# Kernel tuning notes

Hardware: AMD Instinct MI355X
Metric: run time of the kernel (lower is better)

The kernel has to match this reference:

```python
import jax, jax.numpy as jnp
import numpy as np

N_NODES = 100000
N_EDGES = 1600000
IN_DIM = 128
HID = 128
OUT = 40


def setup_inputs() -> dict:
    key = jax.random.key(0)
    ks = jax.random.split(key, 8)
    x = jax.random.normal(ks[0], (N_NODES, IN_DIM), dtype=jnp.float32)
    edge_index = jax.random.randint(ks[1], (2, N_EDGES), 0, N_NODES, dtype=jnp.int64)
    def glorot(k, fan_in, fan_out):
        s = jnp.sqrt(6.0 / (fan_in + fan_out)).astype(jnp.float32)
        return jax.random.uniform(k, (fan_in, fan_out), jnp.float32, -s, s)
    return {
        "x": x,
        "edge_index": edge_index,
        "W1": glorot(ks[2], IN_DIM, HID), "b1": jnp.zeros((HID,), jnp.float32),
        "W2": glorot(ks[3], HID, HID),    "b2": jnp.zeros((HID,), jnp.float32),
        "W3": glorot(ks[4], HID, HID),    "b3": jnp.zeros((HID,), jnp.float32),
        "Wl": glorot(ks[5], HID, OUT),    "bl": jnp.zeros((OUT,), jnp.float32),
    }


def _gcn_norm(edge_index, num_nodes):
    # PyG GCNConv default: add self-loops, symmetric normalization.
    loops = jnp.arange(num_nodes, dtype=edge_index.dtype)
    src = jnp.concatenate([edge_index[0], loops])
    dst = jnp.concatenate([edge_index[1], loops])
    deg = jax.ops.segment_sum(jnp.ones_like(dst, dtype=jnp.float32), dst,
                              num_segments=num_nodes)
    dis = jnp.where(deg > 0, jax.lax.rsqrt(deg), 0.0)  # deg^{-1/2}
    norm = dis[src] * dis[dst]  # [E+N]
    return src, dst, norm


def _gcn_conv(x, W, b, src, dst, norm, num_nodes):
    h = x @ W                                   # [N, F_out]
    msg = h[src] * norm[:, None]                # gather + scale
    out = jax.ops.segment_sum(msg, dst, num_segments=num_nodes)
    return out + b


def reference(x, edge_index, W1, b1, W2, b2, W3, b3, Wl, bl):
    n = x.shape[0]
    src, dst, norm = _gcn_norm(edge_index, n)
    h = jax.nn.relu(_gcn_conv(x, W1, b1, src, dst, norm, n))
    h = jax.nn.relu(_gcn_conv(h, W2, b2, src, dst, norm, n))
    h = _gcn_conv(h, W3, b3, src, dst, norm, n)
    # dropout p=0.5 is identity in eval mode
    return h @ Wl + bl
```

## Files before the change

### kernel.cpp

```cpp
#include <hip/hip_runtime.h>

typedef __attribute__((ext_vector_type(8))) short sh8;
typedef __attribute__((ext_vector_type(4))) float f4;

__device__ __forceinline__ float bf2f(unsigned short u) {
    union { unsigned int u; float f; } c; c.u = ((unsigned int)u) << 16; return c.f;
}
__device__ __forceinline__ unsigned short f2bf(float f) {
    union { float f; unsigned int u; } c; c.f = f;
    unsigned int x = c.u;
    unsigned int r = (x + 0x7fffu + ((x >> 16) & 1u)) >> 16;
    return (unsigned short)r;
}
__device__ __forceinline__ void bfsplit(float x, short& hi, short& lo) {
    unsigned short h = f2bf(x);
    float r = x - bf2f(h);
    hi = (short)h;
    lo = (short)f2bf(r);
}

__global__ void k_zero_cnt(int* cnt, int N) {
    int i = blockIdx.x * 256 + threadIdx.x;
    if (i < N) cnt[i] = 0;
}

__global__ void k_count(const int* __restrict__ dst, int* __restrict__ cnt, int E, int N) {
    int g = blockIdx.x & 7;
    int j = blockIdx.x >> 3;
    int nb = gridDim.x >> 3;
    int lo = (int)((long long)g * N / 8);
    int hi = (int)((long long)(g + 1) * N / 8);
    for (int e = j * 256 + threadIdx.x; e < E; e += nb * 256) {
        int d = dst[e];
        if (d >= lo && d < hi) atomicAdd(&cnt[d], 1);
    }
}

#define SCAN_B 256
__global__ void k_scan_a(const int* __restrict__ cnt, int* __restrict__ rowptr,
                         int* __restrict__ bsum, float* __restrict__ dis, int N) {
    __shared__ int sh[SCAN_B];
    int t = threadIdx.x, i = blockIdx.x * SCAN_B + t;
    int v = (i < N) ? cnt[i] : 0;
    if (i < N) dis[i] = rsqrtf((float)(v + 1));
    sh[t] = v; __syncthreads();
    for (int off = 1; off < SCAN_B; off <<= 1) {
        int x = (t >= off) ? sh[t - off] : 0;
        __syncthreads();
        sh[t] += x;
        __syncthreads();
    }
    int incl = sh[t];
    if (i < N) rowptr[i] = incl - v;
    if (t == SCAN_B - 1) bsum[blockIdx.x] = incl;
}

__global__ void k_scan_b(int* bsum, int NB) {
    __shared__ int sh[512];
    int t = threadIdx.x;
    int v = (t < NB) ? bsum[t] : 0;
    sh[t] = v; __syncthreads();
    for (int off = 1; off < 512; off <<= 1) {
        int x = (t >= off) ? sh[t - off] : 0;
        __syncthreads();
        sh[t] += x;
        __syncthreads();
    }
    if (t < NB) bsum[t] = sh[t] - v;
}

__global__ void k_scan_c(int* __restrict__ rowptr, int* __restrict__ cursor,
                         const int* __restrict__ bsum, int N) {
    int i = blockIdx.x * 256 + threadIdx.x;
    if (i < N) {
        int r = rowptr[i] + bsum[blockIdx.x];
        rowptr[i] = r;
        cursor[i] = r;
    }
}

__global__ void k_fill(const int* __restrict__ src, const int* __restrict__ dst,
                       int* __restrict__ cursor, int* __restrict__ csrc, int E, int N) {
    int g = blockIdx.x & 7;
    int j = blockIdx.x >> 3;
    int nb = gridDim.x >> 3;
    int lo = (int)((long long)g * N / 8);
    int hi = (int)((long long)(g + 1) * N / 8);
    for (int e = j * 256 + threadIdx.x; e < E; e += nb * 256) {
        int d = dst[e];
        if (d < lo || d >= hi) continue;
        int s = src[e];
        if ((unsigned)s >= (unsigned)N) continue;
        int p = atomicAdd(&cursor[d], 1);
        csrc[p] = s;
    }
}

__global__ __launch_bounds__(256)
void k_gemm128_a32(const float* __restrict__ X,
                   const float* __restrict__ W,
                   unsigned short* __restrict__ H, int nPairs) {
    int wave = threadIdx.x >> 6;
    int lane = threadIdx.x & 63;
    int ln = lane & 15, quad = lane >> 4;
    int c0 = (wave & 1) * 64;
    int subTile = wave >> 1;

    sh8 bh[4][4], blo[4][4];
    #pragma unroll
    for (int nt = 0; nt < 4; ++nt) {
        int col = c0 + nt * 16 + ln;
        #pragma unroll
        for (int kt = 0; kt < 4; ++kt) {
            int k0 = kt * 32 + quad * 8;
            #pragma unroll
            for (int j = 0; j < 8; ++j) {
                short h, l;
                bfsplit(W[(k0 + j) * 128 + col], h, l);
                bh[nt][kt][j] = h; blo[nt][kt][j] = l;
            }
        }
    }

    for (int p = blockIdx.x; p < nPairs; p += gridDim.x) {
        int nodeBase = p * 32 + subTile * 16;
        const float* xrow = X + (nodeBase + ln) * 128 + quad * 8;
        sh8 ah[4], al[4];
        #pragma unroll
        for (int kt = 0; kt < 4; ++kt) {
            f4 v0 = *(const f4*)(xrow + kt * 32);
            f4 v1 = *(const f4*)(xrow + kt * 32 + 4);
            #pragma unroll
            for (int j = 0; j < 4; ++j) {
                short h, l;
                bfsplit(v0[j], h, l); ah[kt][j] = h; al[kt][j] = l;
                bfsplit(v1[j], h, l); ah[kt][j + 4] = h; al[kt][j + 4] = l;
            }
        }

        f4 acc[4] = { {0.f,0.f,0.f,0.f}, {0.f,0.f,0.f,0.f}, {0.f,0.f,0.f,0.f}, {0.f,0.f,0.f,0.f} };
        #pragma unroll
        for (int kt = 0; kt < 4; ++kt)
            #pragma unroll
            for (int nt = 0; nt < 4; ++nt) {
                acc[nt] = __builtin_amdgcn_mfma_f32_16x16x32_bf16(ah[kt], bh[nt][kt], acc[nt], 0, 0, 0);
                acc[nt] = __builtin_amdgcn_mfma_f32_16x16x32_bf16(ah[kt], blo[nt][kt], acc[nt], 0, 0, 0);
                acc[nt] = __builtin_amdgcn_mfma_f32_16x16x32_bf16(al[kt], bh[nt][kt], acc[nt], 0, 0, 0);
            }

        #pragma unroll
        for (int nt = 0; nt < 4; ++nt) {
            int col = c0 + nt * 16 + ln;
            #pragma unroll
            for (int r = 0; r < 4; ++r)
                H[(nodeBase + quad * 4 + r) * 128 + col] = f2bf(acc[nt][r]);
        }
    }
}

__global__ __launch_bounds__(256)
void k_gemm128_a16(const unsigned short* __restrict__ X,
                   const float* __restrict__ W,
                   unsigned short* __restrict__ H, int nPairs) {
    int wave = threadIdx.x >> 6;
    int lane = threadIdx.x & 63;
    int ln = lane & 15, quad = lane >> 4;
    int c0 = (wave & 1) * 64;
    int subTile = wave >> 1;

    sh8 bh[4][4], blo[4][4];
    #pragma unroll
    for (int nt = 0; nt < 4; ++nt) {
        int col = c0 + nt * 16 + ln;
        #pragma unroll
        for (int kt = 0; kt < 4; ++kt) {
            int k0 = kt * 32 + quad * 8;
            #pragma unroll
            for (int j = 0; j < 8; ++j) {
                short h, l;
                bfsplit(W[(k0 + j) * 128 + col], h, l);
                bh[nt][kt][j] = h; blo[nt][kt][j] = l;
            }
        }
    }

    for (int p = blockIdx.x; p < nPairs; p += gridDim.x) {
        int nodeBase = p * 32 + subTile * 16;
        const unsigned short* xrow = X + (nodeBase + ln) * 128 + quad * 8;
        sh8 a[4];
        #pragma unroll
        for (int kt = 0; kt < 4; ++kt) a[kt] = *(const sh8*)(xrow + kt * 32);

        f4 acc[4] = { {0.f,0.f,0.f,0.f}, {0.f,0.f,0.f,0.f}, {0.f,0.f,0.f,0.f}, {0.f,0.f,0.f,0.f} };
        #pragma unroll
        for (int kt = 0; kt < 4; ++kt)
            #pragma unroll
            for (int nt = 0; nt < 4; ++nt) {
                acc[nt] = __builtin_amdgcn_mfma_f32_16x16x32_bf16(a[kt], bh[nt][kt], acc[nt], 0, 0, 0);
                acc[nt] = __builtin_amdgcn_mfma_f32_16x16x32_bf16(a[kt], blo[nt][kt], acc[nt], 0, 0, 0);
            }

        #pragma unroll
        for (int nt = 0; nt < 4; ++nt) {
            int col = c0 + nt * 16 + ln;
            #pragma unroll
            for (int r = 0; r < 4; ++r)
                H[(nodeBase + quad * 4 + r) * 128 + col] = f2bf(acc[nt][r]);
        }
    }
}

__global__ __launch_bounds__(256)
void k_agg(const unsigned short* __restrict__ H,
           unsigned short* __restrict__ O,
           const float* __restrict__ dis,
           const int* __restrict__ rowptr,
           const int* __restrict__ cnt,
           const int* __restrict__ csrc,
           const float* __restrict__ bias,
           int relu, int N) {
    int n = (blockIdx.x * 256 + threadIdx.x) >> 6;
    int lane = threadIdx.x & 63;
    if (n >= N) return;
    int c = lane * 2;

    float dn = dis[n];
    unsigned int hv = *(const unsigned int*)(H + n * 128 + c);
    float a0 = bf2f((unsigned short)hv) * dn * dn;
    float a1 = bf2f((unsigned short)(hv >> 16)) * dn * dn;

    int start = rowptr[n];
    int e = cnt[n];
    int i = 0;
    for (; i + 8 <= e; i += 8) {
        int s[8];
        #pragma unroll
        for (int q = 0; q < 8; ++q) s[q] = csrc[start + i + q];
        unsigned int v[8];
        #pragma unroll
        for (int q = 0; q < 8; ++q) v[q] = *(const unsigned int*)(H + (size_t)s[q] * 128 + c);
        float w[8];
        #pragma unroll
        for (int q = 0; q < 8; ++q) w[q] = dis[s[q]] * dn;
        #pragma unroll
        for (int q = 0; q < 8; ++q) {
            a0 += w[q] * bf2f((unsigned short)v[q]);
            a1 += w[q] * bf2f((unsigned short)(v[q] >> 16));
        }
    }
    if (i + 4 <= e) {
        int s[4];
        #pragma unroll
        for (int q = 0; q < 4; ++q) s[q] = csrc[start + i + q];
        unsigned int v[4];
        #pragma unroll
        for (int q = 0; q < 4; ++q) v[q] = *(const unsigned int*)(H + (size_t)s[q] * 128 + c);
        #pragma unroll
        for (int q = 0; q < 4; ++q) {
            float w = dis[s[q]] * dn;
            a0 += w * bf2f((unsigned short)v[q]);
            a1 += w * bf2f((unsigned short)(v[q] >> 16));
        }
        i += 4;
    }
    for (; i < e; ++i) {
        int s0 = csrc[start + i];
        unsigned int v0 = *(const unsigned int*)(H + (size_t)s0 * 128 + c);
        float w0 = dis[s0] * dn;
        a0 += w0 * bf2f((unsigned short)v0);
        a1 += w0 * bf2f((unsigned short)(v0 >> 16));
    }

    a0 += bias[c];
    a1 += bias[c + 1];
    if (relu) { a0 = fmaxf(a0, 0.f); a1 = fmaxf(a1, 0.f); }

    unsigned int ov = (unsigned int)f2bf(a0) | ((unsigned int)f2bf(a1) << 16);
    *(unsigned int*)(O + n * 128 + c) = ov;
}

__global__ __launch_bounds__(256)
void k_gemm_final(const unsigned short* __restrict__ X,
                  const float* __restrict__ W,
                  const float* __restrict__ bl,
                  float* __restrict__ OUT, int nTiles) {
    int wave = threadIdx.x >> 6;
    int lane = threadIdx.x & 63;
    int ln = lane & 15, quad = lane >> 4;
    int tile = blockIdx.x * 4 + wave;
    if (tile >= nTiles) return;

    sh8 bh[3][4], blo[3][4];
    #pragma unroll
    for (int nt = 0; nt < 3; ++nt) {
        int col = nt * 16 + ln;
        bool valid = (col < 40);
        #pragma unroll
        for (int kt = 0; kt < 4; ++kt) {
            int k0 = kt * 32 + quad * 8;
            #pragma unroll
            for (int j = 0; j < 8; ++j) {
                short h = 0, l = 0;
                if (valid) bfsplit(W[(k0 + j) * 40 + col], h, l);
                bh[nt][kt][j] = h; blo[nt][kt][j] = l;
            }
        }
    }

    int nodeBase = tile * 16;
    const unsigned short* xrow = X + (nodeBase + ln) * 128 + quad * 8;
    sh8 a[4];
    #pragma unroll
    for (int kt = 0; kt < 4; ++kt) a[kt] = *(const sh8*)(xrow + kt * 32);

    f4 acc[3] = { {0.f,0.f,0.f,0.f}, {0.f,0.f,0.f,0.f}, {0.f,0.f,0.f,0.f} };
    #pragma unroll
    for (int kt = 0; kt < 4; ++kt)
        #pragma unroll
        for (int nt = 0; nt < 3; ++nt) {
            acc[nt] = __builtin_amdgcn_mfma_f32_16x16x32_bf16(a[kt], bh[nt][kt], acc[nt], 0, 0, 0);
            acc[nt] = __builtin_amdgcn_mfma_f32_16x16x32_bf16(a[kt], blo[nt][kt], acc[nt], 0, 0, 0);
        }

    #pragma unroll
    for (int nt = 0; nt < 3; ++nt) {
        int col = nt * 16 + ln;
        if (col < 40) {
            float bv = bl[col];
            #pragma unroll
            for (int r = 0; r < 4; ++r)
                OUT[(nodeBase + quad * 4 + r) * 40 + col] = acc[nt][r] + bv;
        }
    }
}

extern "C" void kernel_launch(void* const* d_in, const int* in_sizes, int n_in,
                              void* d_out, int out_size, void* d_ws, size_t ws_size,
                              hipStream_t stream) {
    const float* x  = (const float*)d_in[0];
    const int*   ei = (const int*)d_in[1];
    const float* W1 = (const float*)d_in[2];
    const float* b1 = (const float*)d_in[3];
    const float* W2 = (const float*)d_in[4];
    const float* b2 = (const float*)d_in[5];
    const float* W3 = (const float*)d_in[6];
    const float* b3 = (const float*)d_in[7];
    const float* Wl = (const float*)d_in[8];
    const float* bl = (const float*)d_in[9];

    const int N = in_sizes[0] / 128;
    const int E = in_sizes[1] / 2;
    const int* srcIdx = ei;
    const int* dstIdx = ei + E;

    char* ws = (char*)d_ws;
    size_t off = 0;
    auto alloc = [&](size_t bytes) { void* p = ws + off; off += (bytes + 511) & ~(size_t)511; return p; };
    int*   cnt     = (int*)  alloc((size_t)N * 4);
    int*   rowptr  = (int*)  alloc((size_t)N * 4);
    int*   cursor  = (int*)  alloc((size_t)N * 4);
    float* dis     = (float*)alloc((size_t)N * 4);
    int*   bsum    = (int*)  alloc(512 * 4);
    int*   csrc    = (int*)  alloc((size_t)E * 4);
    unsigned short* h0 = (unsigned short*)alloc((size_t)N * 128 * 2);
    unsigned short* h1 = (unsigned short*)alloc((size_t)N * 128 * 2);

    const int gN = (N + 255) / 256;
    const int nPairs = N / 32;
    const int nTiles = N / 16;
    const int gAgg = (N * 64) / 256;
    const int gPart = 1024;

    k_zero_cnt<<<gN, 256, 0, stream>>>(cnt, N);
    k_count<<<gPart, 256, 0, stream>>>(dstIdx, cnt, E, N);
    k_scan_a<<<gN, 256, 0, stream>>>(cnt, rowptr, bsum, dis, N);
    k_scan_b<<<1, 512, 0, stream>>>(bsum, gN);
    k_scan_c<<<gN, 256, 0, stream>>>(rowptr, cursor, bsum, N);
    k_fill<<<gPart, 256, 0, stream>>>(srcIdx, dstIdx, cursor, csrc, E, N);

    k_gemm128_a32<<<768, 256, 0, stream>>>(x, W1, h0, nPairs);
    k_agg<<<gAgg, 256, 0, stream>>>(h0, h1, dis, rowptr, cnt, csrc, b1, 1, N);
    k_gemm128_a16<<<768, 256, 0, stream>>>(h1, W2, h0, nPairs);
    k_agg<<<gAgg, 256, 0, stream>>>(h0, h1, dis, rowptr, cnt, csrc, b2, 1, N);
    k_gemm128_a16<<<768, 256, 0, stream>>>(h1, W3, h0, nPairs);
    k_agg<<<gAgg, 256, 0, stream>>>(h0, h1, dis, rowptr, cnt, csrc, b3, 0, N);
    k_gemm_final<<<(nTiles + 3) / 4, 256, 0, stream>>>(h1, Wl, bl, (float*)d_out, nTiles);
}
```

Before: 549.7 us.

## Use XCD-affine work queues for CSR build and split aggregation across half-waves

The count and fill kernels now pull chunks of edges from per-destination-range atomic queues. Each block starts with the range matching its own XCD, read through a hardware register, so atomics on a given node range tend to stay in one XCD's L2 rather than relying on a fixed blockIdx mapping. The aggregation kernel now has each half-wave handle alternate edges with 8-byte loads covering 4 features, then combines the halves with a shuffle. This doubles the number of gathers in flight per row. The costs are queue-atomic and syncthreads overhead, plus a dependence on the XCD hardware-register encoding; the source-index bounds check in fill was also dropped.

New measurement: 772.2 us. +40.5%, slower.

```diff
diff --git a/kernel.cpp b/kernel.cpp
--- a/kernel.cpp
+++ b/kernel.cpp
@@ -18,21 +18,39 @@
     hi = (short)h;
     lo = (short)f2bf(r);
 }
-
-__global__ void k_zero_cnt(int* cnt, int N) {
+__device__ __forceinline__ int my_xcd() {
+    return (int)(__builtin_amdgcn_s_getreg(63508) & 7u);
+}
+
+#define FILL_CH 4096
+
+__global__ void k_zero_cnt(int* cnt, int* queues, int N) {
     int i = blockIdx.x * 256 + threadIdx.x;
     if (i < N) cnt[i] = 0;
-}
-
-__global__ void k_count(const int* __restrict__ dst, int* __restrict__ cnt, int E, int N) {
-    int g = blockIdx.x & 7;
-    int j = blockIdx.x >> 3;
-    int nb = gridDim.x >> 3;
-    int lo = (int)((long long)g * N / 8);
-    int hi = (int)((long long)(g + 1) * N / 8);
-    for (int e = j * 256 + threadIdx.x; e < E; e += nb * 256) {
-        int d = dst[e];
-        if (d >= lo && d < hi) atomicAdd(&cnt[d], 1);
+    if (blockIdx.x == 0 && threadIdx.x < 16) queues[threadIdx.x] = 0;
+}
+
+__global__ void k_count(const int* __restrict__ dst, int* __restrict__ cnt,
+                        int* __restrict__ queue, int E, int N, int nChunks) {
+    __shared__ int sT;
+    int xcd = my_xcd();
+    for (int gi = 0; gi < 8; ++gi) {
+        int gg = (xcd + gi) & 7;
+        int lo = (int)((long long)gg * N / 8);
+        int hi = (int)((long long)(gg + 1) * N / 8);
+        for (;;) {
+            if (threadIdx.x == 0) sT = atomicAdd(&queue[gg], 1);
+            __syncthreads();
+            int t = sT;
+            __syncthreads();
+            if (t >= nChunks) break;
+            int base = t * FILL_CH;
+            int end = base + FILL_CH; if (end > E) end = E;
+            for (int e = base + threadIdx.x; e < end; e += 256) {
+                int d = dst[e];
+                if (d >= lo && d < hi) atomicAdd(&cnt[d], 1);
+            }
+        }
     }
 }
 
@@ -80,19 +98,30 @@
 }
 
 __global__ void k_fill(const int* __restrict__ src, const int* __restrict__ dst,
-                       int* __restrict__ cursor, int* __restrict__ csrc, int E, int N) {
-    int g = blockIdx.x & 7;
-    int j = blockIdx.x >> 3;
-    int nb = gridDim.x >> 3;
-    int lo = (int)((long long)g * N / 8);
-    int hi = (int)((long long)(g + 1) * N / 8);
-    for (int e = j * 256 + threadIdx.x; e < E; e += nb * 256) {
-        int d = dst[e];
-        if (d < lo || d >= hi) continue;
-        int s = src[e];
-        if ((unsigned)s >= (unsigned)N) continue;
-        int p = atomicAdd(&cursor[d], 1);
-        csrc[p] = s;
+                       int* __restrict__ cursor, int* __restrict__ csrc,
+                       int* __restrict__ queue, int E, int N, int nChunks) {
+    __shared__ int sT;
+    int xcd = my_xcd();
+    for (int gi = 0; gi < 8; ++gi) {
+        int gg = (xcd + gi) & 7;
+        int lo = (int)((long long)gg * N / 8);
+        int hi = (int)((long long)(gg + 1) * N / 8);
+        for (;;) {
+            if (threadIdx.x == 0) sT = atomicAdd(&queue[gg], 1);
+            __syncthreads();
+            int t = sT;
+            __syncthreads();
+            if (t >= nChunks) break;
+            int base = t * FILL_CH;
+            int end = base + FILL_CH; if (end > E) end = E;
+            for (int e = base + threadIdx.x; e < end; e += 256) {
+                int d = dst[e];
+                if (d < lo || d >= hi) continue;
+                int s = src[e];
+                int p = atomicAdd(&cursor[d], 1);
+                csrc[p] = s;
+            }
+        }
     }
 }
 
@@ -222,61 +251,82 @@
     int n = (blockIdx.x * 256 + threadIdx.x) >> 6;
     int lane = threadIdx.x & 63;
     if (n >= N) return;
-    int c = lane * 2;
+    int half = lane >> 5;
+    int sl = lane & 31;
 
     float dn = dis[n];
-    unsigned int hv = *(const unsigned int*)(H + n * 128 + c);
-    float a0 = bf2f((unsigned short)hv) * dn * dn;
-    float a1 = bf2f((unsigned short)(hv >> 16)) * dn * dn;
+    float a0 = 0.f, a1 = 0.f, a2 = 0.f, a3 = 0.f;
+
+    if (half == 0) {
+        uint2 v = *(const uint2*)(H + (size_t)n * 128 + sl * 4);
+        float w = dn * dn;
+        a0 += w * bf2f((unsigned short)v.x);
+        a1 += w * bf2f((unsigned short)(v.x >> 16));
+        a2 += w * bf2f((unsigned short)v.y);
+        a3 += w * bf2f((unsigned short)(v.y >> 16));
+    }
 
     int start = rowptr[n];
     int e = cnt[n];
+    int ePair = e & ~1;
     int i = 0;
-    for (; i + 8 <= e; i += 8) {
-        int s[8];
-        #pragma unroll
-        for (int q = 0; q < 8; ++q) s[q] = csrc[start + i + q];
-        unsigned int v[8];
-        #pragma unroll
-        for (int q = 0; q < 8; ++q) v[q] = *(const unsigned int*)(H + (size_t)s[q] * 128 + c);
-        float w[8];
-        #pragma unroll
-        for (int q = 0; q < 8; ++q) w[q] = dis[s[q]] * dn;
-        #pragma unroll
-        for (int q = 0; q < 8; ++q) {
-            a0 += w[q] * bf2f((unsigned short)v[q]);
-            a1 += w[q] * bf2f((unsigned short)(v[q] >> 16));
-        }
-    }
-    if (i + 4 <= e) {
+    for (; i + 8 <= ePair; i += 8) {
         int s[4];
         #pragma unroll
-        for (int q = 0; q < 4; ++q) s[q] = csrc[start + i + q];
-        unsigned int v[4];
-        #pragma unroll
-        for (int q = 0; q < 4; ++q) v[q] = *(const unsigned int*)(H + (size_t)s[q] * 128 + c);
+        for (int q = 0; q < 4; ++q) s[q] = csrc[start + i + 2 * q + half];
+        uint2 v[4];
+        #pragma unroll
+        for (int q = 0; q < 4; ++q) v[q] = *(const uint2*)(H + (size_t)s[q] * 128 + sl * 4);
+        float w[4];
+        #pragma unroll
+        for (int q = 0; q < 4; ++q) w[q] = dis[s[q]] * dn;
         #pragma unroll
         for (int q = 0; q < 4; ++q) {
-            float w = dis[s[q]] * dn;
-            a0 += w * bf2f((unsigned short)v[q]);
-            a1 += w * bf2f((unsigned short)(v[q] >> 16));
-        }
-        i += 4;
-    }
-    for (; i < e; ++i) {
-        int s0 = csrc[start + i];
-        unsigned int v0 = *(const unsigned int*)(H + (size_t)s0 * 128 + c);
-        float w0 = dis[s0] * dn;
-        a0 += w0 * bf2f((unsigned short)v0);
-        a1 += w0 * bf2f((unsigned short)(v0 >> 16));
-    }
-
-    a0 += bias[c];
-    a1 += bias[c + 1];
-    if (relu) { a0 = fmaxf(a0, 0.f); a1 = fmaxf(a1, 0.f); }
-
-    unsigned int ov = (unsigned int)f2bf(a0) | ((unsigned int)f2bf(a1) << 16);
-    *(unsigned int*)(O + n * 128 + c) = ov;
+            a0 += w[q] * bf2f((unsigned short)v[q].x);
+            a1 += w[q] * bf2f((unsigned short)(v[q].x >> 16));
+            a2 += w[q] * bf2f((unsigned short)v[q].y);
+            a3 += w[q] * bf2f((unsigned short)(v[q].y >> 16));
+        }
+    }
+    for (; i < ePair; i += 2) {
+        int s0 = csrc[start + i + half];
+        uint2 v = *(const uint2*)(H + (size_t)s0 * 128 + sl * 4);
+        float w = dis[s0] * dn;
+        a0 += w * bf2f((unsigned short)v.x);
+        a1 += w * bf2f((unsigned short)(v.x >> 16));
+        a2 += w * bf2f((unsigned short)v.y);
+        a3 += w * bf2f((unsigned short)(v.y >> 16));
+    }
+    if ((e & 1) && half == 0) {
+        int s0 = csrc[start + e - 1];
+        uint2 v = *(const uint2*)(H + (size_t)s0 * 128 + sl * 4);
+        float w = dis[s0] * dn;
+        a0 += w * bf2f((unsigned short)v.x);
+        a1 += w * bf2f((unsigned short)(v.x >> 16));
+        a2 += w * bf2f((unsigned short)v.y);
+        a3 += w * bf2f((unsigned short)(v.y >> 16));
+    }
+
+    a0 += __shfl_down(a0, 32);
+    a1 += __shfl_down(a1, 32);
+    a2 += __shfl_down(a2, 32);
+    a3 += __shfl_down(a3, 32);
+
+    if (half == 0) {
+        int c = sl * 4;
+        a0 += bias[c];
+        a1 += bias[c + 1];
+        a2 += bias[c + 2];
+        a3 += bias[c + 3];
+        if (relu) {
+            a0 = fmaxf(a0, 0.f); a1 = fmaxf(a1, 0.f);
+            a2 = fmaxf(a2, 0.f); a3 = fmaxf(a3, 0.f);
+        }
+        uint2 ov;
+        ov.x = (unsigned int)f2bf(a0) | ((unsigned int)f2bf(a1) << 16);
+        ov.y = (unsigned int)f2bf(a2) | ((unsigned int)f2bf(a3) << 16);
+        *(uint2*)(O + (size_t)n * 128 + c) = ov;
+    }
 }
 
 __global__ __launch_bounds__(256)
@@ -361,6 +411,7 @@
     int*   cursor  = (int*)  alloc((size_t)N * 4);
     float* dis     = (float*)alloc((size_t)N * 4);
     int*   bsum    = (int*)  alloc(512 * 4);
+    int*   queues  = (int*)  alloc(16 * 4);
     int*   csrc    = (int*)  alloc((size_t)E * 4);
     unsigned short* h0 = (unsigned short*)alloc((size_t)N * 128 * 2);
     unsigned short* h1 = (unsigned short*)alloc((size_t)N * 128 * 2);
@@ -370,13 +421,14 @@
     const int nTiles = N / 16;
     const int gAgg = (N * 64) / 256;
     const int gPart = 1024;
-
-    k_zero_cnt<<<gN, 256, 0, stream>>>(cnt, N);
-    k_count<<<gPart, 256, 0, stream>>>(dstIdx, cnt, E, N);
+    const int nChunks = (E + FILL_CH - 1) / FILL_CH;
+
+    k_zero_cnt<<<gN, 256, 0, stream>>>(cnt, queues, N);
+    k_count<<<gPart, 256, 0, stream>>>(dstIdx, cnt, queues, E, N, nChunks);
     k_scan_a<<<gN, 256, 0, stream>>>(cnt, rowptr, bsum, dis, N);
     k_scan_b<<<1, 512, 0, stream>>>(bsum, gN);
     k_scan_c<<<gN, 256, 0, stream>>>(rowptr, cursor, bsum, N);
-    k_fill<<<gPart, 256, 0, stream>>>(srcIdx, dstIdx, cursor, csrc, E, N);
+    k_fill<<<gPart, 256, 0, stream>>>(srcIdx, dstIdx, cursor, csrc, queues + 8, E, N, nChunks);
 
     k_gemm128_a32<<<768, 256, 0, stream>>>(x, W1, h0, nPairs);
     k_agg<<<gAgg, 256, 0, stream>>>(h0, h1, dis, rowptr, cnt, csrc, b1, 1, N);
```
